# Kernel tuning notes

Measured on AMD Instinct MI355X. Metric: run time of the kernel, lower is better.

Reference implementation:

```python
import jax, jax.numpy as jnp
import numpy as np


def setup_inputs() -> dict:
    key = jax.random.key(0)
    k1, k2, k3, k4 = jax.random.split(key, 4)
    B, Nq, Nk, D = 8, 2048, 2048, 768
    return {
        "query": jax.random.normal(k1, (B, Nq, D), dtype=jnp.float32),
        "key": jax.random.normal(k2, (Nk, D), dtype=jnp.float32),
        "x": jax.random.normal(k3, (B, Nk, D), dtype=jnp.float32),
        "W": jax.random.normal(k4, (D, D), dtype=jnp.float32) * (1.0 / np.sqrt(D)),
        "b": jnp.zeros((D,), dtype=jnp.float32),
    }


def reference(query, key, x, W, b):
    # Linear projection: [B,Nq,dk] @ W^T + b -> [B,Nq,dq]
    query_proj = jnp.einsum("bqd,ed->bqe", query, W) + b
    # tensordot over dim_query: [B,Nq,dq] x [Nk,dq] -> [B,Nq,Nk]
    score = jnp.einsum("bqe,ke->bqk", query_proj, key)
    attn = jax.nn.softmax(score, axis=-1)
    # bmm: [B,Nq,Nk] @ [B,Nk,Dv] -> [B,Nq,Dv]
    out = jnp.einsum("bqk,bkd->bqd", attn, x)
    return (out, attn)
```

## Files before the change

kernel.cpp:

```cpp
#include <hip/hip_runtime.h>

typedef short s16x8 __attribute__((ext_vector_type(8)));
typedef float f32x4 __attribute__((ext_vector_type(4)));

__device__ __forceinline__ unsigned short f2bf(float f) {
    unsigned int u = __builtin_bit_cast(unsigned int, f);
    u += 0x7FFFu + ((u >> 16) & 1u);
    return (unsigned short)(u >> 16);
}
__device__ __forceinline__ float bf2f(unsigned short h) {
    unsigned int u = ((unsigned int)h) << 16;
    return __builtin_bit_cast(float, u);
}

__device__ __forceinline__ int swz(int row, int kbyte) {
    return (row * 64 + kbyte) ^ (((row >> 1) & 3) << 4);
}

__device__ __forceinline__ void gl16(const void* g, void* l) {
    __builtin_amdgcn_global_load_lds(
        (__attribute__((address_space(1))) void*)(g),
        (__attribute__((address_space(3))) void*)(l), 16, 0, 0);
}

template<int SPLIT, bool TRANSB, bool BIAS>
__global__ __launch_bounds__(256, 1) void mfma_gemm(
    const float* __restrict__ A, const float* __restrict__ Bsrc,
    const float* __restrict__ bias, float* __restrict__ C,
    int M, int N, int K, long strideA, long strideB, long strideC)
{
    constexpr int NB = (SPLIT > 1) ? 2 : 1;
    __shared__ unsigned short sA[NB][128 * 32];
    __shared__ unsigned short sB[NB][128 * 32];

    const int t  = threadIdx.x;
    const int bz = blockIdx.z;
    const float* Ab = A    + (long)bz * strideA;
    const float* Bb = Bsrc + (long)bz * strideB;
    float*       Cb = C    + (long)bz * strideC;
    const int m0 = blockIdx.y * 128;
    const int n0 = blockIdx.x * 128;

    const int l  = t & 63, w = t >> 6;
    const int rm = (w >> 1) * 64;
    const int cn = (w & 1) * 64;
    const int lr = l & 15;
    const int kg = (l >> 4) * 16;

    const int srow = t >> 1;
    const int skh  = (t & 1) * 16;
    const int s_ = t & 15;
    const int kp = t >> 4;

    f32x4 acc[4][4];
    #pragma unroll
    for (int i = 0; i < 4; ++i)
        #pragma unroll
        for (int j = 0; j < 4; ++j)
            acc[i][j] = (f32x4){0.f, 0.f, 0.f, 0.f};

    for (int kt = 0; kt < K; kt += 32) {
        {
            const float* p = &Ab[(long)(m0 + srow) * K + kt + skh];
            float f[16];
            #pragma unroll
            for (int q = 0; q < 4; ++q) {
                const float4 v = *(const float4*)(p + 4 * q);
                f[4*q+0] = v.x; f[4*q+1] = v.y; f[4*q+2] = v.z; f[4*q+3] = v.w;
            }
            s16x8 h0, h1, l0, l1;
            #pragma unroll
            for (int q = 0; q < 8; ++q) {
                unsigned short h = f2bf(f[q]);      h0[q] = (short)h;
                if (SPLIT > 1) l0[q] = (short)f2bf(f[q] - bf2f(h));
                unsigned short g = f2bf(f[8 + q]);  h1[q] = (short)g;
                if (SPLIT > 1) l1[q] = (short)f2bf(f[8 + q] - bf2f(g));
            }
            *(s16x8*)((char*)sA[0] + swz(srow, skh * 2))      = h0;
            *(s16x8*)((char*)sA[0] + swz(srow, skh * 2 + 16)) = h1;
            if (SPLIT > 1) {
                *(s16x8*)((char*)sA[1] + swz(srow, skh * 2))      = l0;
                *(s16x8*)((char*)sA[1] + swz(srow, skh * 2 + 16)) = l1;
            }
        }
        if (!TRANSB) {
            const float* p = &Bb[(long)(n0 + srow) * K + kt + skh];
            float f[16];
            #pragma unroll
            for (int q = 0; q < 4; ++q) {
                const float4 v = *(const float4*)(p + 4 * q);
                f[4*q+0] = v.x; f[4*q+1] = v.y; f[4*q+2] = v.z; f[4*q+3] = v.w;
            }
            s16x8 h0, h1, l0, l1;
            #pragma unroll
            for (int q = 0; q < 8; ++q) {
                unsigned short h = f2bf(f[q]);      h0[q] = (short)h;
                if (SPLIT > 1) l0[q] = (short)f2bf(f[q] - bf2f(h));
                unsigned short g = f2bf(f[8 + q]);  h1[q] = (short)g;
                if (SPLIT > 1) l1[q] = (short)f2bf(f[8 + q] - bf2f(g));
            }
            *(s16x8*)((char*)sB[0] + swz(srow, skh * 2))      = h0;
            *(s16x8*)((char*)sB[0] + swz(srow, skh * 2 + 16)) = h1;
            if (SPLIT > 1) {
                *(s16x8*)((char*)sB[1] + swz(srow, skh * 2))      = l0;
                *(s16x8*)((char*)sB[1] + swz(srow, skh * 2 + 16)) = l1;
            }
        } else {
            const float* r0 = &Bb[(long)(kt + 2 * kp) * N + n0 + s_ * 8];
            const float* r1 = r0 + N;
            float a0[8], a1[8];
            {
                const float4 u0 = *(const float4*)(r0);
                const float4 u1 = *(const float4*)(r0 + 4);
                const float4 v0 = *(const float4*)(r1);
                const float4 v1 = *(const float4*)(r1 + 4);
                a0[0]=u0.x;a0[1]=u0.y;a0[2]=u0.z;a0[3]=u0.w;
                a0[4]=u1.x;a0[5]=u1.y;a0[6]=u1.z;a0[7]=u1.w;
                a1[0]=v0.x;a1[1]=v0.y;a1[2]=v0.z;a1[3]=v0.w;
                a1[4]=v1.x;a1[5]=v1.y;a1[6]=v1.z;a1[7]=v1.w;
            }
            #pragma unroll
            for (int j = 0; j < 8; ++j) {
                const int i  = (j + s_) & 7;
                const int nl = s_ * 8 + i;
                const unsigned int val =
                    (unsigned int)f2bf(a0[i]) | ((unsigned int)f2bf(a1[i]) << 16);
                *(unsigned int*)((char*)sB[0] + swz(nl, 4 * kp)) = val;
            }
        }
        __syncthreads();

        s16x8 ah[4], bh[4];
        #pragma unroll
        for (int mi = 0; mi < 4; ++mi)
            ah[mi] = *(const s16x8*)((const char*)sA[0] + swz(rm + mi * 16 + lr, kg));
        #pragma unroll
        for (int nj = 0; nj < 4; ++nj)
            bh[nj] = *(const s16x8*)((const char*)sB[0] + swz(cn + nj * 16 + lr, kg));
        #pragma unroll
        for (int mi = 0; mi < 4; ++mi)
            #pragma unroll
            for (int nj = 0; nj < 4; ++nj)
                acc[mi][nj] = __builtin_amdgcn_mfma_f32_16x16x32_bf16(
                    ah[mi], bh[nj], acc[mi][nj], 0, 0, 0);
        if (SPLIT > 1) {
            s16x8 al[4], bl[4];
            #pragma unroll
            for (int mi = 0; mi < 4; ++mi)
                al[mi] = *(const s16x8*)((const char*)sA[1] + swz(rm + mi * 16 + lr, kg));
            #pragma unroll
            for (int mi = 0; mi < 4; ++mi)
                #pragma unroll
                for (int nj = 0; nj < 4; ++nj)
                    acc[mi][nj] = __builtin_amdgcn_mfma_f32_16x16x32_bf16(
                        al[mi], bh[nj], acc[mi][nj], 0, 0, 0);
            #pragma unroll
            for (int nj = 0; nj < 4; ++nj)
                bl[nj] = *(const s16x8*)((const char*)sB[1] + swz(cn + nj * 16 + lr, kg));
            #pragma unroll
            for (int mi = 0; mi < 4; ++mi)
                #pragma unroll
                for (int nj = 0; nj < 4; ++nj)
                    acc[mi][nj] = __builtin_amdgcn_mfma_f32_16x16x32_bf16(
                        ah[mi], bl[nj], acc[mi][nj], 0, 0, 0);
        }
        __syncthreads();
    }

    #pragma unroll
    for (int mi = 0; mi < 4; ++mi) {
        #pragma unroll
        for (int nj = 0; nj < 4; ++nj) {
            const int row = m0 + rm + mi * 16 + (l >> 4) * 4;
            const int col = n0 + cn + nj * 16 + lr;
            const float badd = BIAS ? bias[col] : 0.f;
            #pragma unroll
            for (int r = 0; r < 4; ++r)
                Cb[(long)(row + r) * N + col] = acc[mi][nj][r] + badd;
        }
    }
}

__global__ __launch_bounds__(256, 1) void score_gemm(
    const unsigned short* __restrict__ Ah, const unsigned short* __restrict__ Al,
    const unsigned short* __restrict__ Bh, const unsigned short* __restrict__ Bl,
    const float* __restrict__ bias, float* __restrict__ C,
    int M, int N, int K, int nbx)
{
    __shared__ unsigned short sAh[128 * 32];
    __shared__ unsigned short sBh[128 * 32];
    __shared__ unsigned short sAl[128 * 32];
    __shared__ unsigned short sBl[128 * 32];

    const int bid = blockIdx.x;
    const int cpx = gridDim.x >> 3;
    const int sw  = (bid & 7) * cpx + (bid >> 3);
    const int mb  = sw / nbx, nb = sw % nbx;
    const int m0 = mb * 128, n0 = nb * 128;

    const int t = threadIdx.x;
    const int l = t & 63, w = t >> 6;
    const int rm = (w >> 1) * 64;
    const int cn = (w & 1) * 64;
    const int lr = l & 15;
    const int kg = (l >> 4) * 16;

    const int r0 = 2 * w, r1 = 2 * w + 1;
    const int rowS0 = 16 * r0 + (l >> 2);
    const int rowS1 = 16 * r1 + (l >> 2);
    const int h0 = (l & 3) ^ ((rowS0 >> 1) & 3);
    const int h1 = (l & 3) ^ ((rowS1 >> 1) & 3);

    const unsigned short* gAh0 = Ah + (long)(m0 + rowS0) * K + 8 * h0;
    const unsigned short* gAh1 = Ah + (long)(m0 + rowS1) * K + 8 * h1;
    const unsigned short* gAl0 = Al + (long)(m0 + rowS0) * K + 8 * h0;
    const unsigned short* gAl1 = Al + (long)(m0 + rowS1) * K + 8 * h1;
    const unsigned short* gBh0 = Bh + (long)(n0 + rowS0) * K + 8 * h0;
    const unsigned short* gBh1 = Bh + (long)(n0 + rowS1) * K + 8 * h1;
    const unsigned short* gBl0 = Bl + (long)(n0 + rowS0) * K + 8 * h0;
    const unsigned short* gBl1 = Bl + (long)(n0 + rowS1) * K + 8 * h1;

    unsigned short* dA0 = &sAh[r0 * 512];
    unsigned short* dA1 = &sAh[r1 * 512];
    unsigned short* dAl0 = &sAl[r0 * 512];
    unsigned short* dAl1 = &sAl[r1 * 512];
    unsigned short* dB0 = &sBh[r0 * 512];
    unsigned short* dB1 = &sBh[r1 * 512];
    unsigned short* dBl0 = &sBl[r0 * 512];
    unsigned short* dBl1 = &sBl[r1 * 512];

    f32x4 acc[4][4];
    #pragma unroll
    for (int i = 0; i < 4; ++i)
        #pragma unroll
        for (int j = 0; j < 4; ++j)
            acc[i][j] = (f32x4){0.f, 0.f, 0.f, 0.f};

    const int nk = K >> 5;
    for (int it = 0; it < nk; ++it) {
        gl16(gAh0, dA0);  gl16(gAh1, dA1);
        gl16(gBh0, dB0);  gl16(gBh1, dB1);
        gl16(gAl0, dAl0); gl16(gAl1, dAl1);
        gl16(gBl0, dBl0); gl16(gBl1, dBl1);
        gAh0 += 32; gAh1 += 32; gAl0 += 32; gAl1 += 32;
        gBh0 += 32; gBh1 += 32; gBl0 += 32; gBl1 += 32;
        __syncthreads();

        s16x8 ah[4], bh[4];
        #pragma unroll
        for (int mi = 0; mi < 4; ++mi)
            ah[mi] = *(const s16x8*)((const char*)sAh + swz(rm + mi * 16 + lr, kg));
        #pragma unroll
        for (int nj = 0; nj < 4; ++nj)
            bh[nj] = *(const s16x8*)((const char*)sBh + swz(cn + nj * 16 + lr, kg));
        #pragma unroll
        for (int mi = 0; mi < 4; ++mi)
            #pragma unroll
            for (int nj = 0; nj < 4; ++nj)
                acc[mi][nj] = __builtin_amdgcn_mfma_f32_16x16x32_bf16(
                    ah[mi], bh[nj], acc[mi][nj], 0, 0, 0);
        s16x8 al[4], bl[4];
        #pragma unroll
        for (int mi = 0; mi < 4; ++mi)
            al[mi] = *(const s16x8*)((const char*)sAl + swz(rm + mi * 16 + lr, kg));
        #pragma unroll
        for (int mi = 0; mi < 4; ++mi)
            #pragma unroll
            for (int nj = 0; nj < 4; ++nj)
                acc[mi][nj] = __builtin_amdgcn_mfma_f32_16x16x32_bf16(
                    al[mi], bh[nj], acc[mi][nj], 0, 0, 0);
        #pragma unroll
        for (int nj = 0; nj < 4; ++nj)
            bl[nj] = *(const s16x8*)((const char*)sBl + swz(cn + nj * 16 + lr, kg));
        #pragma unroll
        for (int mi = 0; mi < 4; ++mi)
            #pragma unroll
            for (int nj = 0; nj < 4; ++nj)
                acc[mi][nj] = __builtin_amdgcn_mfma_f32_16x16x32_bf16(
                    ah[mi], bl[nj], acc[mi][nj], 0, 0, 0);
        __syncthreads();
    }

    #pragma unroll
    for (int mi = 0; mi < 4; ++mi) {
        #pragma unroll
        for (int nj = 0; nj < 4; ++nj) {
            const int row = m0 + rm + mi * 16 + (l >> 4) * 4;
            const int col = n0 + cn + nj * 16 + lr;
            const float badd = bias[col];
            #pragma unroll
            for (int r = 0; r < 4; ++r)
                C[(long)(row + r) * N + col] = acc[mi][nj][r] + badd;
        }
    }
}

__global__ __launch_bounds__(256, 1) void out_gemm(
    const float* __restrict__ A32, const unsigned short* __restrict__ B16,
    float* __restrict__ C, int M, int N, int K,
    long strideA, long strideB, long strideC)
{
    __shared__ unsigned short sA[128 * 32];
    __shared__ unsigned short sB[128 * 32];

    const int bz = blockIdx.z;
    const float* Ab = A32 + (long)bz * strideA;
    const unsigned short* Bb = B16 + (long)bz * strideB;
    float* Cb = C + (long)bz * strideC;
    const int m0 = blockIdx.x * 128;
    const int n0 = blockIdx.y * 128;

    const int t = threadIdx.x;
    const int l = t & 63, w = t >> 6;
    const int rm = (w >> 1) * 64;
    const int cn = (w & 1) * 64;
    const int lr = l & 15;
    const int kg = (l >> 4) * 16;

    const int r0 = 2 * w, r1 = 2 * w + 1;
    const int rowS0 = 16 * r0 + (l >> 2);
    const int rowS1 = 16 * r1 + (l >> 2);
    const int h0 = (l & 3) ^ ((rowS0 >> 1) & 3);
    const int h1 = (l & 3) ^ ((rowS1 >> 1) & 3);
    const unsigned short* gB0 = Bb + (long)(n0 + rowS0) * K + 8 * h0;
    const unsigned short* gB1 = Bb + (long)(n0 + rowS1) * K + 8 * h1;
    unsigned short* dB0 = &sB[r0 * 512];
    unsigned short* dB1 = &sB[r1 * 512];

    const int srow = t >> 1;
    const int skh  = (t & 1) * 16;
    const float* gA = &Ab[(long)(m0 + srow) * K + skh];

    f32x4 acc[4][4];
    #pragma unroll
    for (int i = 0; i < 4; ++i)
        #pragma unroll
        for (int j = 0; j < 4; ++j)
            acc[i][j] = (f32x4){0.f, 0.f, 0.f, 0.f};

    const int nk = K >> 5;
    for (int it = 0; it < nk; ++it) {
        gl16(gB0, dB0); gl16(gB1, dB1);
        gB0 += 32; gB1 += 32;
        {
            float f[16];
            #pragma unroll
            for (int q = 0; q < 4; ++q) {
                const float4 v = *(const float4*)(gA + 4 * q);
                f[4*q+0] = v.x; f[4*q+1] = v.y; f[4*q+2] = v.z; f[4*q+3] = v.w;
            }
            gA += 32;
            s16x8 v0, v1;
            #pragma unroll
            for (int q = 0; q < 8; ++q) {
                v0[q] = (short)f2bf(f[q]);
                v1[q] = (short)f2bf(f[8 + q]);
            }
            *(s16x8*)((char*)sA + swz(srow, skh * 2))      = v0;
            *(s16x8*)((char*)sA + swz(srow, skh * 2 + 16)) = v1;
        }
        __syncthreads();

        s16x8 ah[4], bh[4];
        #pragma unroll
        for (int mi = 0; mi < 4; ++mi)
            ah[mi] = *(const s16x8*)((const char*)sA + swz(rm + mi * 16 + lr, kg));
        #pragma unroll
        for (int nj = 0; nj < 4; ++nj)
            bh[nj] = *(const s16x8*)((const char*)sB + swz(cn + nj * 16 + lr, kg));
        #pragma unroll
        for (int mi = 0; mi < 4; ++mi)
            #pragma unroll
            for (int nj = 0; nj < 4; ++nj)
                acc[mi][nj] = __builtin_amdgcn_mfma_f32_16x16x32_bf16(
                    ah[mi], bh[nj], acc[mi][nj], 0, 0, 0);
        __syncthreads();
    }

    #pragma unroll
    for (int mi = 0; mi < 4; ++mi) {
        #pragma unroll
        for (int nj = 0; nj < 4; ++nj) {
            const int row = m0 + rm + mi * 16 + (l >> 4) * 4;
            const int col = n0 + cn + nj * 16 + lr;
            #pragma unroll
            for (int r = 0; r < 4; ++r)
                Cb[(long)(row + r) * N + col] = acc[mi][nj][r];
        }
    }
}

template<bool TOBF16>
__global__ __launch_bounds__(256) void transpose64(
    const float* __restrict__ in, void* __restrict__ outv,
    int R, int Cc, long sIn, long sOut)
{
    __shared__ float tl[64][65];
    const int z = blockIdx.z;
    const float* ib = in + (long)z * sIn;
    const int r0 = blockIdx.x * 64, c0 = blockIdx.y * 64;
    const int t = threadIdx.x;
    const int lrr = t >> 4, lc = (t & 15) * 4;
    #pragma unroll
    for (int p = 0; p < 4; ++p) {
        const float4 v = *(const float4*)&ib[(long)(r0 + lrr + 16 * p) * Cc + c0 + lc];
        tl[lrr + 16 * p][lc + 0] = v.x; tl[lrr + 16 * p][lc + 1] = v.y;
        tl[lrr + 16 * p][lc + 2] = v.z; tl[lrr + 16 * p][lc + 3] = v.w;
    }
    __syncthreads();
    #pragma unroll
    for (int p = 0; p < 4; ++p) {
        const int orow = c0 + lrr + 16 * p;
        const int ocol = r0 + lc;
        const float a = tl[lc + 0][lrr + 16 * p];
        const float b = tl[lc + 1][lrr + 16 * p];
        const float c = tl[lc + 2][lrr + 16 * p];
        const float d = tl[lc + 3][lrr + 16 * p];
        if (TOBF16) {
            ushort4 u = { f2bf(a), f2bf(b), f2bf(c), f2bf(d) };
            *(ushort4*)((unsigned short*)outv + (long)z * sOut + (long)orow * R + ocol) = u;
        } else {
            float4 u = { a, b, c, d };
            *(float4*)((float*)outv + (long)z * sOut + (long)orow * R + ocol) = u;
        }
    }
}

__global__ __launch_bounds__(256) void convert_hilo(
    const float* __restrict__ src, unsigned short* __restrict__ hi,
    unsigned short* __restrict__ lo, long n8)
{
    for (long i = (long)blockIdx.x * blockDim.x + threadIdx.x; i < n8;
         i += (long)gridDim.x * blockDim.x) {
        const float4 a = *(const float4*)&src[i * 8];
        const float4 b = *(const float4*)&src[i * 8 + 4];
        const float f[8] = { a.x, a.y, a.z, a.w, b.x, b.y, b.z, b.w };
        s16x8 h, lv;
        #pragma unroll
        for (int q = 0; q < 8; ++q) {
            const unsigned short hh = f2bf(f[q]);
            h[q]  = (short)hh;
            lv[q] = (short)f2bf(f[q] - bf2f(hh));
        }
        *(s16x8*)&hi[i * 8] = h;
        *(s16x8*)&lo[i * 8] = lv;
    }
}

__global__ __launch_bounds__(256) void bk_dot(
    const float* __restrict__ key, const float* __restrict__ b,
    float* __restrict__ bk, int D)
{
    const int row = blockIdx.x * 4 + (threadIdx.x >> 6);
    const int l = threadIdx.x & 63;
    const float* kr = key + (long)row * D;
    float s = 0.f;
    for (int e = l; e < D; e += 64) s += kr[e] * b[e];
    #pragma unroll
    for (int off = 32; off > 0; off >>= 1) s += __shfl_xor(s, off);
    if (l == 0) bk[row] = s;
}

__global__ __launch_bounds__(256) void softmax_rows(float* __restrict__ S, int cols)
{
    const long row = blockIdx.x;
    float* p = S + row * (long)cols;
    const int t = threadIdx.x;
    const int wid = t >> 6;

    float vals[8];
    float m = -INFINITY;
    #pragma unroll
    for (int i = 0; i < 8; ++i) {
        vals[i] = p[t + i * 256];
        m = fmaxf(m, vals[i]);
    }
    #pragma unroll
    for (int off = 32; off > 0; off >>= 1)
        m = fmaxf(m, __shfl_xor(m, off));
    __shared__ float smax[4], ssum[4];
    if ((t & 63) == 0) smax[wid] = m;
    __syncthreads();
    m = fmaxf(fmaxf(smax[0], smax[1]), fmaxf(smax[2], smax[3]));

    float s = 0.f;
    #pragma unroll
    for (int i = 0; i < 8; ++i) {
        vals[i] = __expf(vals[i] - m);
        s += vals[i];
    }
    #pragma unroll
    for (int off = 32; off > 0; off >>= 1)
        s += __shfl_xor(s, off);
    if ((t & 63) == 0) ssum[wid] = s;
    __syncthreads();
    s = (ssum[0] + ssum[1]) + (ssum[2] + ssum[3]);
    const float inv = 1.0f / s;
    #pragma unroll
    for (int i = 0; i < 8; ++i)
        p[t + i * 256] = vals[i] * inv;
}

extern "C" void kernel_launch(void* const* d_in, const int* in_sizes, int n_in,
                              void* d_out, int out_size, void* d_ws, size_t ws_size,
                              hipStream_t stream)
{
    const float* query = (const float*)d_in[0];
    const float* key   = (const float*)d_in[1];
    const float* x     = (const float*)d_in[2];
    const float* W     = (const float*)d_in[3];
    const float* bias  = (const float*)d_in[4];

    const int D  = in_sizes[4];
    const int Nk = in_sizes[1] / D;
    const int B  = in_sizes[2] / (Nk * D);
    const int Nq = in_sizes[0] / (B * D);

    float* out  = (float*)d_out;
    float* attn = out + (long)B * Nq * D;

    const long nQ  = (long)B * Nq * D;
    const long nKW = (long)Nk * D;
    const size_t wsNeed = (size_t)nQ * 2 * 2;

    if (ws_size >= wsNeed) {
        unsigned short* q_hi  = (unsigned short*)out;
        unsigned short* KW_hi = q_hi + nQ;
        unsigned short* KW_lo = KW_hi + nKW;
        float*          bk    = (float*)(KW_lo + nKW);
        unsigned short* q_lo  = (unsigned short*)d_ws;
        unsigned short* xT    = q_lo + nQ;
        float* Wt  = attn;
        float* KWf = attn + 1048576;

        dim3 gtw(D / 64, D / 64, 1);
        transpose64<false><<<gtw, 256, 0, stream>>>(W, Wt, D, D, 0L, 0L);
        dim3 gkw(D / 128, Nk / 128, 1);
        mfma_gemm<3, false, false><<<gkw, 256, 0, stream>>>(
            key, Wt, nullptr, KWf, Nk, D, D, 0L, 0L, 0L);
        convert_hilo<<<768, 256, 0, stream>>>(KWf, KW_hi, KW_lo, nKW / 8);
        bk_dot<<<Nk / 4, 256, 0, stream>>>(key, bias, bk, D);
        convert_hilo<<<2048, 256, 0, stream>>>(query, q_hi, q_lo, nQ / 8);
        dim3 gtx(Nk / 64, D / 64, B);
        transpose64<true><<<gtx, 256, 0, stream>>>(
            x, xT, Nk, D, (long)Nk * D, (long)D * Nk);
        const int nbx = Nk / 128;
        const int nwg = (B * Nq / 128) * nbx;
        score_gemm<<<nwg, 256, 0, stream>>>(
            q_hi, q_lo, KW_hi, KW_lo, bk, attn, B * Nq, Nk, D, nbx);
        softmax_rows<<<B * Nq, 256, 0, stream>>>(attn, Nk);
        dim3 go(Nq / 128, D / 128, B);
        out_gemm<<<go, 256, 0, stream>>>(
            attn, xT, out, Nq, D, Nk, (long)Nq * Nk, (long)D * Nk, (long)Nq * D);
    } else {
        float* qp = out;
        dim3 g1(D / 128, (B * Nq) / 128, 1);
        mfma_gemm<3, false, true><<<g1, 256, 0, stream>>>(
            query, W, bias, qp, B * Nq, D, D, 0L, 0L, 0L);
        dim3 g2(Nk / 128, Nq / 128, B);
        mfma_gemm<3, false, false><<<g2, 256, 0, stream>>>(
            qp, key, nullptr, attn, Nq, Nk, D, (long)Nq * D, 0L, (long)Nq * Nk);
        softmax_rows<<<B * Nq, 256, 0, stream>>>(attn, Nk);
        dim3 g4(D / 128, Nq / 128, B);
        mfma_gemm<1, true, false><<<g4, 256, 0, stream>>>(
            attn, x, nullptr, out, Nq, D, Nk, (long)Nq * Nk, (long)Nk * D, (long)Nq * D);
    }
}
```

Measured before the change: 383.6 us.

## Emit bf16 attention copy from softmax and feed a bf16-only output GEMM

The softmax kernel now uses vectorized float4 loads and stores and also writes a bf16 copy of the attention matrix to workspace. A new out_gemm2 reads that bf16 attention directly through global-to-LDS loads, so the output GEMM no longer reads fp32 attention and converts it in-kernel. This path runs only when the workspace can hold the transposed x plus the bf16 attention buffer, and it adds an extra bf16 write of the full attention matrix.

```diff
diff --git a/kernel.cpp b/kernel.cpp
--- a/kernel.cpp
+++ b/kernel.cpp
@@ -295,6 +295,86 @@
     }
 }
 
+__global__ __launch_bounds__(256, 1) void out_gemm2(
+    const unsigned short* __restrict__ A16, const unsigned short* __restrict__ B16,
+    float* __restrict__ C, int M, int N, int K,
+    long strideA, long strideB, long strideC)
+{
+    __shared__ unsigned short sA[128 * 32];
+    __shared__ unsigned short sB[128 * 32];
+
+    const int bz = blockIdx.z;
+    const unsigned short* Ab = A16 + (long)bz * strideA;
+    const unsigned short* Bb = B16 + (long)bz * strideB;
+    float* Cb = C + (long)bz * strideC;
+    const int m0 = blockIdx.x * 128;
+    const int n0 = blockIdx.y * 128;
+
+    const int t = threadIdx.x;
+    const int l = t & 63, w = t >> 6;
+    const int rm = (w >> 1) * 64;
+    const int cn = (w & 1) * 64;
+    const int lr = l & 15;
+    const int kg = (l >> 4) * 16;
+
+    const int r0 = 2 * w, r1 = 2 * w + 1;
+    const int rowS0 = 16 * r0 + (l >> 2);
+    const int rowS1 = 16 * r1 + (l >> 2);
+    const int h0 = (l & 3) ^ ((rowS0 >> 1) & 3);
+    const int h1 = (l & 3) ^ ((rowS1 >> 1) & 3);
+
+    const unsigned short* gA0 = Ab + (long)(m0 + rowS0) * K + 8 * h0;
+    const unsigned short* gA1 = Ab + (long)(m0 + rowS1) * K + 8 * h1;
+    const unsigned short* gB0 = Bb + (long)(n0 + rowS0) * K + 8 * h0;
+    const unsigned short* gB1 = Bb + (long)(n0 + rowS1) * K + 8 * h1;
+    unsigned short* dA0 = &sA[r0 * 512];
+    unsigned short* dA1 = &sA[r1 * 512];
+    unsigned short* dB0 = &sB[r0 * 512];
+    unsigned short* dB1 = &sB[r1 * 512];
+
+    f32x4 acc[4][4];
+    #pragma unroll
+    for (int i = 0; i < 4; ++i)
+        #pragma unroll
+        for (int j = 0; j < 4; ++j)
+            acc[i][j] = (f32x4){0.f, 0.f, 0.f, 0.f};
+
+    const int nk = K >> 5;
+    for (int it = 0; it < nk; ++it) {
+        gl16(gA0, dA0); gl16(gA1, dA1);
+        gl16(gB0, dB0); gl16(gB1, dB1);
+        gA0 += 32; gA1 += 32; gB0 += 32; gB1 += 32;
+        __syncthreads();
+
+        s16x8 ah[4], bh[4];
+        #pragma unroll
+        for (int mi = 0; mi < 4; ++mi)
+            ah[mi] = *(const s16x8*)((const char*)sA + swz(rm + mi * 16 + lr, kg));
+        #pragma unroll
+        for (int nj = 0; nj < 4; ++nj)
+            bh[nj] = *(const s16x8*)((const char*)sB + swz(cn + nj * 16 + lr, kg));
+        #pragma unroll
+        for (int mi = 0; mi < 4; ++mi)
+            #pragma unroll
+            for (int nj = 0; nj < 4; ++nj)
+                acc[mi][nj] = __builtin_amdgcn_mfma_f32_16x16x32_bf16(
+                    ah[mi], bh[nj], acc[mi][nj], 0, 0, 0);
+        __syncthreads();
+    }
+
+    #pragma unroll
+    for (int mi = 0; mi < 4; ++mi) {
+        #pragma unroll
+        for (int nj = 0; nj < 4; ++nj) {
+            const int row = m0 + rm + mi * 16 + (l >> 4) * 4;
+            const int col = n0 + cn + nj * 16 + lr;
+            #pragma unroll
+            for (int r = 0; r < 4; ++r)
+                Cb[(long)(row + r) * N + col] = acc[mi][nj][r];
+        }
+    }
+}
+
 __global__ __launch_bounds__(256, 1) void out_gemm(
     const float* __restrict__ A32, const unsigned short* __restrict__ B16,
     float* __restrict__ C, int M, int N, int K,
@@ -461,20 +541,22 @@
     if (l == 0) bk[row] = s;
 }
 
-__global__ __launch_bounds__(256) void softmax_rows(float* __restrict__ S, int cols)
+__global__ __launch_bounds__(256) void softmax_bf16(
+    float* __restrict__ S, unsigned short* __restrict__ S16, int cols)
 {
     const long row = blockIdx.x;
     float* p = S + row * (long)cols;
+    unsigned short* p16 = S16 + row * (long)cols;
     const int t = threadIdx.x;
     const int wid = t >> 6;
-
-    float vals[8];
+    const int base = t * 8;
+
+    const float4 a = *(const float4*)&p[base];
+    const float4 b = *(const float4*)&p[base + 4];
+    float vals[8] = { a.x, a.y, a.z, a.w, b.x, b.y, b.z, b.w };
     float m = -INFINITY;
     #pragma unroll
-    for (int i = 0; i < 8; ++i) {
-        vals[i] = p[t + i * 256];
-        m = fmaxf(m, vals[i]);
-    }
+    for (int i = 0; i < 8; ++i) m = fmaxf(m, vals[i]);
     #pragma unroll
     for (int off = 32; off > 0; off >>= 1)
         m = fmaxf(m, __shfl_xor(m, off));
@@ -496,6 +578,53 @@
     __syncthreads();
     s = (ssum[0] + ssum[1]) + (ssum[2] + ssum[3]);
     const float inv = 1.0f / s;
+
+    float4 o0, o1;
+    o0.x = vals[0]*inv; o0.y = vals[1]*inv; o0.z = vals[2]*inv; o0.w = vals[3]*inv;
+    o1.x = vals[4]*inv; o1.y = vals[5]*inv; o1.z = vals[6]*inv; o1.w = vals[7]*inv;
+    *(float4*)&p[base]     = o0;
+    *(float4*)&p[base + 4] = o1;
+    s16x8 h;
+    h[0]=(short)f2bf(o0.x); h[1]=(short)f2bf(o0.y); h[2]=(short)f2bf(o0.z); h[3]=(short)f2bf(o0.w);
+    h[4]=(short)f2bf(o1.x); h[5]=(short)f2bf(o1.y); h[6]=(short)f2bf(o1.z); h[7]=(short)f2bf(o1.w);
+    *(s16x8*)&p16[base] = h;
+}
+
+__global__ __launch_bounds__(256) void softmax_rows(float* __restrict__ S, int cols)
+{
+    const long row = blockIdx.x;
+    float* p = S + row * (long)cols;
+    const int t = threadIdx.x;
+    const int wid = t >> 6;
+
+    float vals[8];
+    float m = -INFINITY;
+    #pragma unroll
+    for (int i = 0; i < 8; ++i) {
+        vals[i] = p[t + i * 256];
+        m = fmaxf(m, vals[i]);
+    }
+    #pragma unroll
+    for (int off = 32; off > 0; off >>= 1)
+        m = fmaxf(m, __shfl_xor(m, off));
+    __shared__ float smax[4], ssum[4];
+    if ((t & 63) == 0) smax[wid] = m;
+    __syncthreads();
+    m = fmaxf(fmaxf(smax[0], smax[1]), fmaxf(smax[2], smax[3]));
+
+    float s = 0.f;
+    #pragma unroll
+    for (int i = 0; i < 8; ++i) {
+        vals[i] = __expf(vals[i] - m);
+        s += vals[i];
+    }
+    #pragma unroll
+    for (int off = 32; off > 0; off >>= 1)
+        s += __shfl_xor(s, off);
+    if ((t & 63) == 0) ssum[wid] = s;
+    __syncthreads();
+    s = (ssum[0] + ssum[1]) + (ssum[2] + ssum[3]);
+    const float inv = 1.0f / s;
     #pragma unroll
     for (int i = 0; i < 8; ++i)
         p[t + i * 256] = vals[i] * inv;
@@ -521,9 +650,46 @@
 
     const long nQ  = (long)B * Nq * D;
     const long nKW = (long)Nk * D;
-    const size_t wsNeed = (size_t)nQ * 2 * 2;
-
-    if (ws_size >= wsNeed) {
+    const long nX  = (long)B * Nk * D;
+    const long nAt = (long)B * Nq * Nk;
+
+    const size_t xTb   = (size_t)nX * 2;
+    const size_t qLob  = (size_t)nQ * 2;
+    const size_t at16b = (size_t)nAt * 2;
+    const size_t wsFull = xTb + (at16b > qLob ? at16b : qLob);
+    const size_t wsMid  = qLob + xTb;
+
+    if (ws_size >= wsFull) {
+        unsigned short* q_hi  = (unsigned short*)out;
+        unsigned short* KW_hi = q_hi + nQ;
+        unsigned short* KW_lo = KW_hi + nKW;
+        float*          bk    = (float*)(KW_lo + nKW);
+        unsigned short* xT     = (unsigned short*)d_ws;
+        unsigned short* q_lo   = (unsigned short*)((char*)d_ws + xTb);
+        unsigned short* attn16 = (unsigned short*)((char*)d_ws + xTb);
+        float* Wt  = attn;
+        float* KWf = attn + 1048576;
+
+        dim3 gtw(D / 64, D / 64, 1);
+        transpose64<false><<<gtw, 256, 0, stream>>>(W, Wt, D, D, 0L, 0L);
+        dim3 gkw(D / 128, Nk / 128, 1);
+        mfma_gemm<3, false, false><<<gkw, 256, 0, stream>>>(
+            key, Wt, nullptr, KWf, Nk, D, D, 0L, 0L, 0L);
+        convert_hilo<<<768, 256, 0, stream>>>(KWf, KW_hi, KW_lo, nKW / 8);
+        bk_dot<<<Nk / 4, 256, 0, stream>>>(key, bias, bk, D);
+        convert_hilo<<<2048, 256, 0, stream>>>(query, q_hi, q_lo, nQ / 8);
+        dim3 gtx(Nk / 64, D / 64, B);
+        transpose64<true><<<gtx, 256, 0, stream>>>(
+            x, xT, Nk, D, (long)Nk * D, (long)D * Nk);
+        const int nbx = Nk / 128;
+        const int nwg = (B * Nq / 128) * nbx;
+        score_gemm<<<nwg, 256, 0, stream>>>(
+            q_hi, q_lo, KW_hi, KW_lo, bk, attn, B * Nq, Nk, D, nbx);
+        softmax_bf16<<<B * Nq, 256, 0, stream>>>(attn, attn16, Nk);
+        dim3 go(Nq / 128, D / 128, B);
+        out_gemm2<<<go, 256, 0, stream>>>(
+            attn16, xT, out, Nq, D, Nk, (long)Nq * Nk, (long)D * Nk, (long)Nq * D);
+    } else if (ws_size >= wsMid) {
         unsigned short* q_hi  = (unsigned short*)out;
         unsigned short* KW_hi = q_hi + nQ;
         unsigned short* KW_lo = KW_hi + nKW;
```

Result: no change. 385.1 us (+0.4%).
